# Kernel tuning notes

Hardware: AMD Instinct MI355X
Metric: run time of the kernel (lower is better)

The kernel has to match this reference:

```python
import jax, jax.numpy as jnp
import numpy as np

D = 768
H = 12
B, T = 2, 2048


def _layernorm(x, g, b, eps=1e-5):
    m = jnp.mean(x, axis=-1, keepdims=True)
    v = jnp.mean((x - m) ** 2, axis=-1, keepdims=True)
    return (x - m) * jax.lax.rsqrt(v + eps) * g + b


def setup_inputs() -> dict:
    key = jax.random.key(0)
    ks = jax.random.split(key, 10)
    s = 0.02
    return {
        "x": jax.random.normal(ks[0], (B, T, D), dtype=jnp.float32),
        "attn_mask": jnp.ones((B, T), dtype=jnp.int32),
        "Wq": jax.random.normal(ks[1], (D, D), dtype=jnp.float32) * s,
        "Wk": jax.random.normal(ks[2], (D, D), dtype=jnp.float32) * s,
        "Wv": jax.random.normal(ks[3], (D, D), dtype=jnp.float32) * s,
        "Wo": jax.random.normal(ks[4], (D, D), dtype=jnp.float32) * s,
        "bo": jnp.zeros((D,), dtype=jnp.float32),
        "ln1_g": jnp.ones((D,), dtype=jnp.float32),
        "ln1_b": jnp.zeros((D,), dtype=jnp.float32),
        "ln2_g": jnp.ones((D,), dtype=jnp.float32),
        "ln2_b": jnp.zeros((D,), dtype=jnp.float32),
        "W1": jax.random.normal(ks[5], (D, 4 * D), dtype=jnp.float32) * s,
        "b1": jnp.zeros((4 * D,), dtype=jnp.float32),
        "W2": jax.random.normal(ks[6], (4 * D, D), dtype=jnp.float32) * s,
        "b2": jnp.zeros((D,), dtype=jnp.float32),
    }


def reference(x, attn_mask, Wq, Wk, Wv, Wo, bo, ln1_g, ln1_b, ln2_g, ln2_b, W1, b1, W2, b2):
    d = x.shape[-1]
    hs = d // H
    # --- multi-head self-attention on ln1(x) ---
    h = _layernorm(x, ln1_g, ln1_b)
    q = jnp.einsum("btd,dhk->bhtk", h, Wq.reshape(d, H, hs))
    k = jnp.einsum("btd,dhk->bhtk", h, Wk.reshape(d, H, hs))
    v = jnp.einsum("btd,dhk->bhtk", h, Wv.reshape(d, H, hs))
    # NOTE: original scales by embed_dim**-0.5 (C = embed_dim), not head_size
    scores = jnp.einsum("bhtk,bhsk->bhts", q, k) * (d ** -0.5)
    key_mask = (attn_mask == 0)[:, None, None, :]  # [B,1,1,T] over key dim
    scores = jnp.where(key_mask, -jnp.inf, scores)
    wei = jax.nn.softmax(scores, axis=-1)
    out = jnp.einsum("bhts,bhsk->bhtk", wei, v)
    out = out.transpose(0, 2, 1, 3).reshape(x.shape)  # concat heads -> [B,T,D]
    x = x + out @ Wo + bo
    # --- feed-forward on ln2(x) ---
    h2 = _layernorm(x, ln2_g, ln2_b)
    ff = jax.nn.relu(h2 @ W1 + b1) @ W2 + b2
    return x + ff
```

## Files before the change

### kernel.cpp

```cpp
#include <hip/hip_runtime.h>


typedef unsigned short u16;
typedef unsigned int u32;
typedef __attribute__((ext_vector_type(8))) short s16x8;
typedef __attribute__((ext_vector_type(4))) float fx4;

#define D_MODEL 768
#define NH 12
#define HS 64
#define TT 2048
#define BB 2

__device__ __forceinline__ u16 f2bf(float f) {
  union { float f; u32 u; } v; v.f = f;
  u32 r = v.u + 0x7fffu + ((v.u >> 16) & 1u);
  return (u16)(r >> 16);
}
__device__ __forceinline__ float bf2f(u16 h) {
  union { u32 u; float f; } v; v.u = ((u32)h) << 16; return v.f;
}

__device__ __forceinline__ void async16(const void* g, void* l) {
  __builtin_amdgcn_global_load_lds(
      (const __attribute__((address_space(1))) u32*)g,
      (__attribute__((address_space(3))) u32*)l, 16, 0, 0);
}

__global__ __launch_bounds__(256) void tconv(const float* __restrict__ in,
                                             u16* __restrict__ out, int R, int C) {
  __shared__ float t[32][33];
  int c0 = blockIdx.x * 32, r0 = blockIdx.y * 32;
  int x = threadIdx.x, y = threadIdx.y;
  for (int i = 0; i < 4; i++)
    t[y + i * 8][x] = in[(size_t)(r0 + y + i * 8) * C + c0 + x];
  __syncthreads();
  for (int i = 0; i < 4; i++)
    out[(size_t)(c0 + y + i * 8) * R + r0 + x] = f2bf(t[x][y + i * 8]);
}

__global__ __launch_bounds__(256) void tconv3(const float* __restrict__ w0,
                                              const float* __restrict__ w1,
                                              const float* __restrict__ w2,
                                              u16* __restrict__ out) {
  __shared__ float t[32][33];
  const float* in = blockIdx.z == 0 ? w0 : blockIdx.z == 1 ? w1 : w2;
  u16* o = out + (size_t)blockIdx.z * 768 * 768;
  int c0 = blockIdx.x * 32, r0 = blockIdx.y * 32;
  int x = threadIdx.x, y = threadIdx.y;
  for (int i = 0; i < 4; i++)
    t[y + i * 8][x] = in[(size_t)(r0 + y + i * 8) * 768 + c0 + x];
  __syncthreads();
  for (int i = 0; i < 4; i++)
    o[(size_t)(c0 + y + i * 8) * 768 + r0 + x] = f2bf(t[x][y + i * 8]);
}

__global__ __launch_bounds__(256) void vt_extract(const u16* __restrict__ qkv,
                                                  u16* __restrict__ vt) {
  __shared__ u16 t[32][33];
  int bh = blockIdx.z, b = bh / NH, h = bh % NH;
  int t0 = blockIdx.x * 32, v0 = blockIdx.y * 32;
  int x = threadIdx.x, y = threadIdx.y;
  for (int i = 0; i < 4; i++)
    t[y + i * 8][x] = qkv[(size_t)(b * TT + t0 + y + i * 8) * 2304 + 1536 + h * HS + v0 + x];
  __syncthreads();
  for (int i = 0; i < 4; i++)
    vt[(size_t)(bh * HS + v0 + y + i * 8) * TT + t0 + x] = t[x][y + i * 8];
}

__global__ __launch_bounds__(256) void maskbias(const int* __restrict__ mask,
                                                float* __restrict__ mb) {
  int i = blockIdx.x * 256 + threadIdx.x;
  mb[i] = mask[i] ? 0.f : -1e30f;
}

__global__ __launch_bounds__(256) void ln_kernel(const float* __restrict__ x,
                                                 const float* __restrict__ g,
                                                 const float* __restrict__ bta,
                                                 u16* __restrict__ out) {
  int row = blockIdx.x;
  const float* xr = x + (size_t)row * D_MODEL;
  int tid = threadIdx.x;
  float v0 = xr[tid], v1 = xr[tid + 256], v2 = xr[tid + 512];
  float s = v0 + v1 + v2, sq = v0 * v0 + v1 * v1 + v2 * v2;
  for (int m = 1; m < 64; m <<= 1) { s += __shfl_xor(s, m); sq += __shfl_xor(sq, m); }
  __shared__ float ss[4], ssq[4];
  int w = tid >> 6;
  if ((tid & 63) == 0) { ss[w] = s; ssq[w] = sq; }
  __syncthreads();
  s = ss[0] + ss[1] + ss[2] + ss[3];
  sq = ssq[0] + ssq[1] + ssq[2] + ssq[3];
  float mean = s * (1.f / D_MODEL);
  float var = sq * (1.f / D_MODEL) - mean * mean;
  float rstd = rsqrtf(var + 1e-5f);
  u16* orow = out + (size_t)row * D_MODEL;
  orow[tid]       = f2bf((v0 - mean) * rstd * g[tid]       + bta[tid]);
  orow[tid + 256] = f2bf((v1 - mean) * rstd * g[tid + 256] + bta[tid + 256]);
  orow[tid + 512] = f2bf((v2 - mean) * rstd * g[tid + 512] + bta[tid + 512]);
}

__global__ __launch_bounds__(256) void red_wo_ln(
    const u16* __restrict__ p0, const u16* __restrict__ p1,
    const u16* __restrict__ p2, const u16* __restrict__ p3,
    const float* __restrict__ x, const float* __restrict__ bo,
    const float* __restrict__ g, const float* __restrict__ be,
    float* __restrict__ yv, u16* __restrict__ h2) {
  int row = blockIdx.x, tid = threadIdx.x;
  size_t base = (size_t)row * D_MODEL;
  float v[3];
  float s = 0.f, sq = 0.f;
  for (int i = 0; i < 3; i++) {
    int c = tid + i * 256;
    size_t idx = base + c;
    float t = bf2f(p0[idx]) + bf2f(p1[idx]) + bf2f(p2[idx]) + bf2f(p3[idx])
            + x[idx] + bo[c];
    v[i] = t; yv[idx] = t;
    s += t; sq += t * t;
  }
  for (int m = 1; m < 64; m <<= 1) { s += __shfl_xor(s, m); sq += __shfl_xor(sq, m); }
  __shared__ float ss[4], ssq[4];
  int w = tid >> 6;
  if ((tid & 63) == 0) { ss[w] = s; ssq[w] = sq; }
  __syncthreads();
  s = ss[0] + ss[1] + ss[2] + ss[3];
  sq = ssq[0] + ssq[1] + ssq[2] + ssq[3];
  float mean = s * (1.f / D_MODEL);
  float var = sq * (1.f / D_MODEL) - mean * mean;
  float rstd = rsqrtf(var + 1e-5f);
  for (int i = 0; i < 3; i++) {
    int c = tid + i * 256;
    h2[base + c] = f2bf((v[i] - mean) * rstd * g[c] + be[c]);
  }
}

__global__ __launch_bounds__(256) void red_ff2(
    const u16* __restrict__ p0, const u16* __restrict__ p1,
    const u16* __restrict__ p2, const float* __restrict__ yv,
    const float* __restrict__ bias, float* __restrict__ out) {
  size_t i = ((size_t)blockIdx.x * 256 + threadIdx.x) * 4;
  int col = (int)(i % D_MODEL);
  ushort4 a = *(const ushort4*)(p0 + i);
  ushort4 b = *(const ushort4*)(p1 + i);
  ushort4 c = *(const ushort4*)(p2 + i);
  float4 y = *(const float4*)(yv + i);
  float4 o;
  o.x = bf2f(a.x) + bf2f(b.x) + bf2f(c.x) + y.x + bias[col];
  o.y = bf2f(a.y) + bf2f(b.y) + bf2f(c.y) + y.y + bias[col + 1];
  o.z = bf2f(a.z) + bf2f(b.z) + bf2f(c.z) + y.z + bias[col + 2];
  o.w = bf2f(a.w) + bf2f(b.w) + bf2f(c.w) + y.w + bias[col + 3];
  *(float4*)(out + i) = o;
}

template <int EPI>
__global__ __launch_bounds__(256) void gemm_bt(
    const u16* __restrict__ A, const u16* __restrict__ Bt,
    int M, int N, int K,
    u16* __restrict__ outb, const float* __restrict__ bias,
    float qs, int qn,
    u16* __restrict__ p0, u16* __restrict__ p1,
    u16* __restrict__ p2, u16* __restrict__ p3) {
  __shared__ __align__(16) u16 lA[128 * 32];
  __shared__ __align__(16) u16 lB[128 * 32];
  const int tid = threadIdx.x;
  const int lane = tid & 63, w = tid >> 6;
  const int quad = lane >> 4, l15 = lane & 15;
  const int wm = w >> 1, wn = w & 1;
  const int bm = blockIdx.y, bn = blockIdx.x;
  const int Ksub = K / gridDim.z;
  const int k0 = blockIdx.z * Ksub;

  fx4 acc[4][4] = {};

  for (int kt = k0; kt < k0 + Ksub; kt += 32) {
    __syncthreads();
    for (int t = 0; t < 2; t++) {
      int p = (w * 2 + t) * 64 + lane;
      int m = p >> 2, qp = p & 3;
      int ql = qp ^ ((m >> 1) & 3);
      async16(A + (size_t)(bm * 128 + m) * K + kt + ql * 8,
              (char*)lA + (w * 2 + t) * 1024);
    }
    for (int t = 0; t < 2; t++) {
      int p = (w * 2 + t) * 64 + lane;
      int n = p >> 2, qp = p & 3;
      int ql = qp ^ ((n >> 1) & 3);
      async16(Bt + (size_t)(bn * 128 + n) * K + kt + ql * 8,
              (char*)lB + (w * 2 + t) * 1024);
    }
    __syncthreads();
    s16x8 af[4], bfr[4];
    for (int i = 0; i < 4; i++) {
      int m = wm * 64 + i * 16 + l15;
      int phys = m * 4 + (quad ^ ((m >> 1) & 3));
      af[i] = *(const s16x8*)((const char*)lA + phys * 16);
    }
    for (int j = 0; j < 4; j++) {
      int n = wn * 64 + j * 16 + l15;
      int phys = n * 4 + (quad ^ ((n >> 1) & 3));
      bfr[j] = *(const s16x8*)((const char*)lB + phys * 16);
    }
    for (int i = 0; i < 4; i++)
      for (int j = 0; j < 4; j++)
        acc[i][j] = __builtin_amdgcn_mfma_f32_16x16x32_bf16(af[i], bfr[j], acc[i][j], 0, 0, 0);
  }

  u16* pb = nullptr;
  if (EPI == 3)
    pb = blockIdx.z == 0 ? p0 : blockIdx.z == 1 ? p1 : blockIdx.z == 2 ? p2 : p3;

  for (int i = 0; i < 4; i++)
    for (int j = 0; j < 4; j++)
      for (int r = 0; r < 4; r++) {
        int row = bm * 128 + wm * 64 + i * 16 + quad * 4 + r;
        int col = bn * 128 + wn * 64 + j * 16 + l15;
        float v = acc[i][j][r];
        if (EPI == 0) {
          float vv = (col < qn) ? v * qs : v;
          outb[(size_t)row * N + col] = f2bf(vv);
        } else if (EPI == 2) {
          outb[(size_t)row * N + col] = f2bf(fmaxf(v + bias[col], 0.f));
        } else {
          pb[(size_t)row * N + col] = f2bf(v);
        }
      }
}

__global__ __launch_bounds__(256) void attn_kernel(
    const u16* __restrict__ qkv, const u16* __restrict__ vt,
    const float* __restrict__ maskadd, u16* __restrict__ out) {
  __shared__ __align__(16) u16 sQ[64 * 64];
  __shared__ __align__(16) u16 sK[64 * 64];
  __shared__ __align__(16) u16 sV[64 * 64];
  __shared__ __align__(16) u16 sP[4][16 * 64];
  const int bh = blockIdx.y, b = bh / NH, h = bh % NH;
  const int qt = blockIdx.x;
  const int tid = threadIdx.x, lane = tid & 63, w = tid >> 6;
  const int quad = lane >> 4, l15 = lane & 15;

  for (int t = 0; t < 2; t++) {
    int p = (w * 2 + t) * 64 + lane;
    int m = p >> 3, qp = p & 7, ql = qp ^ (m & 7);
    async16(qkv + (size_t)(b * TT + qt * 64 + m) * 2304 + h * HS + ql * 8,
            (char*)sQ + (w * 2 + t) * 1024);
  }
  __syncthreads();
  s16x8 aq[2];
  for (int kk = 0; kk < 2; kk++) {
    int m = w * 16 + l15;
    int phys = m * 8 + ((kk * 4 + quad) ^ (m & 7));
    aq[kk] = *(const s16x8*)((const char*)sQ + phys * 16);
  }

  float lsum[4] = {0.f, 0.f, 0.f, 0.f};
  fx4 o[4] = {};

  for (int kc = 0; kc < TT / 64; kc++) {
    __syncthreads();
    for (int t = 0; t < 2; t++) {
      int p = (w * 2 + t) * 64 + lane;
      int m = p >> 3, qp = p & 7, ql = qp ^ (m & 7);
      async16(qkv + (size_t)(b * TT + kc * 64 + m) * 2304 + D_MODEL + h * HS + ql * 8,
              (char*)sK + (w * 2 + t) * 1024);
    }
    for (int t = 0; t < 2; t++) {
      int p = (w * 2 + t) * 64 + lane;
      int m = p >> 3, qp = p & 7, ql = qp ^ (m & 7);
      async16(vt + (size_t)bh * HS * TT + (size_t)m * TT + kc * 64 + ql * 8,
              (char*)sV + (w * 2 + t) * 1024);
    }
    __syncthreads();

    for (int jn = 0; jn < 4; jn++) {
      float mb = maskadd[b * TT + kc * 64 + jn * 16 + l15];
      fx4 s = {mb, mb, mb, mb};
      for (int kk = 0; kk < 2; kk++) {
        int n = jn * 16 + l15;
        int phys = n * 8 + ((kk * 4 + quad) ^ (n & 7));
        s16x8 bk = *(const s16x8*)((const char*)sK + phys * 16);
        s = __builtin_amdgcn_mfma_f32_16x16x32_bf16(aq[kk], bk, s, 0, 0, 0);
      }
      for (int r = 0; r < 4; r++) {
        float p = __builtin_amdgcn_exp2f(s[r]);
        u16 pb = f2bf(p);
        lsum[r] += bf2f(pb);
        int row = quad * 4 + r, k = jn * 16 + l15;
        sP[w][row * 64 + ((k >> 3) ^ (row & 7)) * 8 + (k & 7)] = pb;
      }
    }
    for (int kk = 0; kk < 2; kk++) {
      int m = l15;
      int phys = m * 8 + ((kk * 4 + quad) ^ (m & 7));
      s16x8 ap = *(const s16x8*)((const char*)sP[w] + phys * 16);
      for (int jv = 0; jv < 4; jv++) {
        int n = jv * 16 + l15;
        int ph2 = n * 8 + ((kk * 4 + quad) ^ (n & 7));
        s16x8 bv = *(const s16x8*)((const char*)sV + ph2 * 16);
        o[jv] = __builtin_amdgcn_mfma_f32_16x16x32_bf16(ap, bv, o[jv], 0, 0, 0);
      }
    }
  }

  for (int mm = 1; mm < 16; mm <<= 1)
    for (int r = 0; r < 4; r++) lsum[r] += __shfl_xor(lsum[r], mm);

  for (int jv = 0; jv < 4; jv++)
    for (int r = 0; r < 4; r++) {
      int tok = qt * 64 + w * 16 + quad * 4 + r;
      out[(size_t)(b * TT + tok) * D_MODEL + h * HS + jv * 16 + l15] =
          f2bf(o[jv][r] / lsum[r]);
    }
}

extern "C" void kernel_launch(void* const* d_in, const int* in_sizes, int n_in,
                              void* d_out, int out_size, void* d_ws, size_t ws_size,
                              hipStream_t stream) {
  const float* x    = (const float*)d_in[0];
  const int*   mask = (const int*)d_in[1];
  const float* Wq   = (const float*)d_in[2];
  const float* Wk   = (const float*)d_in[3];
  const float* Wv   = (const float*)d_in[4];
  const float* Wo   = (const float*)d_in[5];
  const float* bo   = (const float*)d_in[6];
  const float* g1   = (const float*)d_in[7];
  const float* be1  = (const float*)d_in[8];
  const float* g2   = (const float*)d_in[9];
  const float* be2  = (const float*)d_in[10];
  const float* W1   = (const float*)d_in[11];
  const float* bb1  = (const float*)d_in[12];
  const float* W2   = (const float*)d_in[13];
  const float* bb2  = (const float*)d_in[14];
  float* out = (float*)d_out;
  char* ws = (char*)d_ws;

  u16*   WqkvT = (u16*)(ws + 0);
  u16*   WoT   = (u16*)(ws + 3538944);
  u16*   W1T   = (u16*)(ws + 4718592);
  u16*   W2T   = (u16*)(ws + 9437184);
  u16*   h1    = (u16*)(ws + 14155776);
  u16*   QKV   = (u16*)(ws + 20447232);
  u16*   Vt    = (u16*)(ws + 39321600);
  u16*   attn  = (u16*)(ws + 45613056);
  float* yv    = (float*)(ws + 51904512);
  float* mbias = yv;
  u16*   h2    = h1;
  u16*   ff1   = QKV;
  u16* pw0 = (u16*)(ws + 20447232);
  u16* pw1 = (u16*)(ws + 26738688);
  u16* pw2 = (u16*)(ws + 33030144);
  u16* pw3 = (u16*)(ws + 39321600);
  u16* pf0 = (u16*)(ws + 0);
  u16* pf1 = (u16*)(ws + 14155776);
  u16* pf2 = (u16*)(ws + 45613056);

  const float QS = 0.05205875399f;

  dim3 tb(32, 8);
  tconv3<<<dim3(24, 24, 3), tb, 0, stream>>>(Wq, Wk, Wv, WqkvT);
  tconv<<<dim3(24, 24), tb, 0, stream>>>(Wo, WoT, 768, 768);
  tconv<<<dim3(96, 24), tb, 0, stream>>>(W1, W1T, 768, 3072);
  tconv<<<dim3(24, 96), tb, 0, stream>>>(W2, W2T, 3072, 768);
  maskbias<<<16, 256, 0, stream>>>(mask, mbias);

  ln_kernel<<<4096, 256, 0, stream>>>(x, g1, be1, h1);
  gemm_bt<0><<<dim3(18, 32, 1), 256, 0, stream>>>(h1, WqkvT, 4096, 2304, 768,
      QKV, nullptr, QS, 768, nullptr, nullptr, nullptr, nullptr);
  vt_extract<<<dim3(64, 2, 24), tb, 0, stream>>>(QKV, Vt);
  attn_kernel<<<dim3(32, 24), 256, 0, stream>>>(QKV, Vt, mbias, attn);
  gemm_bt<3><<<dim3(6, 32, 4), 256, 0, stream>>>(attn, WoT, 4096, 768, 768,
      nullptr, nullptr, 1.f, 0, pw0, pw1, pw2, pw3);
  red_wo_ln<<<4096, 256, 0, stream>>>(pw0, pw1, pw2, pw3, x, bo, g2, be2, yv, h2);
  gemm_bt<2><<<dim3(24, 32, 1), 256, 0, stream>>>(h2, W1T, 4096, 3072, 768,
      ff1, bb1, 1.f, 0, nullptr, nullptr, nullptr, nullptr);
  gemm_bt<3><<<dim3(6, 32, 3), 256, 0, stream>>>(ff1, W2T, 4096, 768, 3072,
      nullptr, nullptr, 1.f, 0, pf0, pf1, pf2, nullptr);
  red_ff2<<<3072, 256, 0, stream>>>(pf0, pf1, pf2, yv, bb2, out);
}
```

Measured before the change: 319.2 us.

## Split attention over key halves and keep P in registers via transposed MFMA

The attention kernel is launched with a second grid dimension over two key halves, which doubles the block count, and each half writes unnormalized partial outputs and row sums. A new reduce kernel then combines and normalizes the halves and transposes the result into the token-major layout. The QK^T product is computed transposed with 16x16x16 bf16 MFMAs so the exponentiated scores feed the PV MFMA directly from registers, removing the shared-memory round trip for P. The mask is also staged in shared memory. The cost is an extra launch plus partial-output traffic, and bf16 rounding of the partial outputs before the sum.

Result: no change. 323.7 us (+1.4%).

```diff
diff --git a/kernel.cpp b/kernel.cpp
--- a/kernel.cpp
+++ b/kernel.cpp
@@ -1,9 +1,11 @@
 #include <hip/hip_runtime.h>
+#include <hip/hip_bf16.h>
 
 
 typedef unsigned short u16;
 typedef unsigned int u32;
 typedef __attribute__((ext_vector_type(8))) short s16x8;
+typedef __attribute__((ext_vector_type(4))) short s16x4;
 typedef __attribute__((ext_vector_type(4))) float fx4;
 
 #define D_MODEL 768
@@ -20,11 +22,22 @@
 __device__ __forceinline__ float bf2f(u16 h) {
   union { u32 u; float f; } v; v.u = ((u32)h) << 16; return v.f;
 }
+__device__ __forceinline__ s16x4 pack4(float a, float b, float c, float d) {
+  union { __hip_bfloat162 h2[2]; s16x4 v; } u;
+  u.h2[0] = __float22bfloat162_rn({a, b});
+  u.h2[1] = __float22bfloat162_rn({c, d});
+  return u.v;
+}
 
 __device__ __forceinline__ void async16(const void* g, void* l) {
   __builtin_amdgcn_global_load_lds(
       (const __attribute__((address_space(1))) u32*)g,
       (__attribute__((address_space(3))) u32*)l, 16, 0, 0);
+}
+
+__device__ __forceinline__ s16x4 lds_rd64(const u16* base, int row, int g) {
+  int a = row * 64 + ((((g >> 1) ^ (row & 7)) << 3) | ((g & 1) << 2));
+  return *(const s16x4*)(base + a);
 }
 
 __global__ __launch_bounds__(256) void tconv(const float* __restrict__ in,
@@ -227,13 +240,14 @@
 
 __global__ __launch_bounds__(256) void attn_kernel(
     const u16* __restrict__ qkv, const u16* __restrict__ vt,
-    const float* __restrict__ maskadd, u16* __restrict__ out) {
+    const float* __restrict__ maskadd,
+    u16* __restrict__ pO0, u16* __restrict__ pO1, float* __restrict__ pL) {
   __shared__ __align__(16) u16 sQ[64 * 64];
   __shared__ __align__(16) u16 sK[64 * 64];
   __shared__ __align__(16) u16 sV[64 * 64];
-  __shared__ __align__(16) u16 sP[4][16 * 64];
+  __shared__ __align__(16) float smask[1024];
   const int bh = blockIdx.y, b = bh / NH, h = bh % NH;
-  const int qt = blockIdx.x;
+  const int qt = blockIdx.x, sp = blockIdx.z;
   const int tid = threadIdx.x, lane = tid & 63, w = tid >> 6;
   const int quad = lane >> 4, l15 = lane & 15;
 
@@ -243,72 +257,91 @@
     async16(qkv + (size_t)(b * TT + qt * 64 + m) * 2304 + h * HS + ql * 8,
             (char*)sQ + (w * 2 + t) * 1024);
   }
-  __syncthreads();
-  s16x8 aq[2];
-  for (int kk = 0; kk < 2; kk++) {
-    int m = w * 16 + l15;
-    int phys = m * 8 + ((kk * 4 + quad) ^ (m & 7));
-    aq[kk] = *(const s16x8*)((const char*)sQ + phys * 16);
-  }
-
-  float lsum[4] = {0.f, 0.f, 0.f, 0.f};
+  for (int j = 0; j < 4; j++)
+    smask[tid + j * 256] = maskadd[b * TT + sp * 1024 + tid + j * 256];
+  __syncthreads();
+
+  s16x4 qb[4];
+  for (int ks = 0; ks < 4; ks++)
+    qb[ks] = lds_rd64(sQ, w * 16 + l15, ks * 4 + quad);
+
+  float lsum = 0.f;
   fx4 o[4] = {};
 
-  for (int kc = 0; kc < TT / 64; kc++) {
+  for (int kc = 0; kc < 16; kc++) {
+    int key0 = sp * 1024 + kc * 64;
     __syncthreads();
     for (int t = 0; t < 2; t++) {
       int p = (w * 2 + t) * 64 + lane;
       int m = p >> 3, qp = p & 7, ql = qp ^ (m & 7);
-      async16(qkv + (size_t)(b * TT + kc * 64 + m) * 2304 + D_MODEL + h * HS + ql * 8,
+      async16(qkv + (size_t)(b * TT + key0 + m) * 2304 + D_MODEL + h * HS + ql * 8,
               (char*)sK + (w * 2 + t) * 1024);
     }
     for (int t = 0; t < 2; t++) {
       int p = (w * 2 + t) * 64 + lane;
       int m = p >> 3, qp = p & 7, ql = qp ^ (m & 7);
-      async16(vt + (size_t)bh * HS * TT + (size_t)m * TT + kc * 64 + ql * 8,
+      async16(vt + (size_t)bh * HS * TT + (size_t)m * TT + key0 + ql * 8,
               (char*)sV + (w * 2 + t) * 1024);
     }
     __syncthreads();
 
-    for (int jn = 0; jn < 4; jn++) {
-      float mb = maskadd[b * TT + kc * 64 + jn * 16 + l15];
-      fx4 s = {mb, mb, mb, mb};
-      for (int kk = 0; kk < 2; kk++) {
-        int n = jn * 16 + l15;
-        int phys = n * 8 + ((kk * 4 + quad) ^ (n & 7));
-        s16x8 bk = *(const s16x8*)((const char*)sK + phys * 16);
-        s = __builtin_amdgcn_mfma_f32_16x16x32_bf16(aq[kk], bk, s, 0, 0, 0);
+    for (int kt = 0; kt < 4; kt++) {
+      float4 mb = *(const float4*)&smask[kc * 64 + kt * 16 + quad * 4];
+      fx4 s = {mb.x, mb.y, mb.z, mb.w};
+      for (int ks = 0; ks < 4; ks++) {
+        s16x4 ak = lds_rd64(sK, kt * 16 + l15, ks * 4 + quad);
+        s = __builtin_amdgcn_mfma_f32_16x16x16bf16_1k(ak, qb[ks], s, 0, 0, 0);
       }
-      for (int r = 0; r < 4; r++) {
-        float p = __builtin_amdgcn_exp2f(s[r]);
-        u16 pb = f2bf(p);
-        lsum[r] += bf2f(pb);
-        int row = quad * 4 + r, k = jn * 16 + l15;
-        sP[w][row * 64 + ((k >> 3) ^ (row & 7)) * 8 + (k & 7)] = pb;
+      float e0 = __builtin_amdgcn_exp2f(s[0]);
+      float e1 = __builtin_amdgcn_exp2f(s[1]);
+      float e2 = __builtin_amdgcn_exp2f(s[2]);
+      float e3 = __builtin_amdgcn_exp2f(s[3]);
+      lsum += (e0 + e1) + (e2 + e3);
+      s16x4 pB = pack4(e0, e1, e2, e3);
+      for (int jv = 0; jv < 4; jv++) {
+        s16x4 av = lds_rd64(sV, jv * 16 + l15, kt * 4 + quad);
+        o[jv] = __builtin_amdgcn_mfma_f32_16x16x16bf16_1k(av, pB, o[jv], 0, 0, 0);
       }
     }
-    for (int kk = 0; kk < 2; kk++) {
-      int m = l15;
-      int phys = m * 8 + ((kk * 4 + quad) ^ (m & 7));
-      s16x8 ap = *(const s16x8*)((const char*)sP[w] + phys * 16);
-      for (int jv = 0; jv < 4; jv++) {
-        int n = jv * 16 + l15;
-        int ph2 = n * 8 + ((kk * 4 + quad) ^ (n & 7));
-        s16x8 bv = *(const s16x8*)((const char*)sV + ph2 * 16);
-        o[jv] = __builtin_amdgcn_mfma_f32_16x16x32_bf16(ap, bv, o[jv], 0, 0, 0);
-      }
-    }
-  }
-
-  for (int mm = 1; mm < 16; mm <<= 1)
-    for (int r = 0; r < 4; r++) lsum[r] += __shfl_xor(lsum[r], mm);
-
+  }
+
+  lsum += __shfl_xor(lsum, 16);
+  lsum += __shfl_xor(lsum, 32);
+
+  const int tile = bh * 32 + qt;
+  u16* po = sp ? pO1 : pO0;
+  size_t base = (size_t)tile * 4096;
   for (int jv = 0; jv < 4; jv++)
     for (int r = 0; r < 4; r++) {
-      int tok = qt * 64 + w * 16 + quad * 4 + r;
-      out[(size_t)(b * TT + tok) * D_MODEL + h * HS + jv * 16 + l15] =
-          f2bf(o[jv][r] / lsum[r]);
-    }
+      int vd = jv * 16 + quad * 4 + r;
+      po[base + vd * 64 + w * 16 + l15] = f2bf(o[jv][r]);
+    }
+  if (quad == 0) pL[sp * 49152 + tile * 64 + w * 16 + l15] = lsum;
+}
+
+__global__ __launch_bounds__(256) void attn_reduce(
+    const u16* __restrict__ pO0, const u16* __restrict__ pO1,
+    const float* __restrict__ pL, u16* __restrict__ out) {
+  __shared__ float T[64 * 65];
+  __shared__ float rinv[64];
+  const int tile = blockIdx.x;
+  const int bh = tile >> 5, qt = tile & 31, b = bh / NH, h = bh % NH;
+  const int t = threadIdx.x;
+  if (t < 64) rinv[t] = 1.f / (pL[tile * 64 + t] + pL[49152 + tile * 64 + t]);
+  __syncthreads();
+  size_t base = (size_t)tile * 4096;
+  for (int i = 0; i < 16; i++) {
+    int idx = i * 256 + t, vd = idx >> 6, q = idx & 63;
+    T[vd * 65 + q] = (bf2f(pO0[base + idx]) + bf2f(pO1[base + idx])) * rinv[q];
+  }
+  __syncthreads();
+  int q = t >> 2, vb = (t & 3) * 16;
+  u16* orow = out + (size_t)(b * TT + qt * 64 + q) * D_MODEL + h * HS + vb;
+  for (int i = 0; i < 8; i++) {
+    int vd = vb + i * 2;
+    u32 pk = (u32)f2bf(T[vd * 65 + q]) | ((u32)f2bf(T[(vd + 1) * 65 + q]) << 16);
+    *(u32*)(orow + i * 2) = pk;
+  }
 }
 
 extern "C" void kernel_launch(void* const* d_in, const int* in_sizes, int n_in,
@@ -342,6 +375,9 @@
   u16*   attn  = (u16*)(ws + 45613056);
   float* yv    = (float*)(ws + 51904512);
   float* mbias = yv;
+  u16*   pO0   = h1;
+  u16*   pO1   = (u16*)(ws + 51920896);
+  float* pL    = (float*)(ws + 58212352);
   u16*   h2    = h1;
   u16*   ff1   = QKV;
   u16* pw0 = (u16*)(ws + 20447232);
@@ -365,7 +401,8 @@
   gemm_bt<0><<<dim3(18, 32, 1), 256, 0, stream>>>(h1, WqkvT, 4096, 2304, 768,
       QKV, nullptr, QS, 768, nullptr, nullptr, nullptr, nullptr);
   vt_extract<<<dim3(64, 2, 24), tb, 0, stream>>>(QKV, Vt);
-  attn_kernel<<<dim3(32, 24), 256, 0, stream>>>(QKV, Vt, mbias, attn);
+  attn_kernel<<<dim3(32, 24, 2), 256, 0, stream>>>(QKV, Vt, mbias, pO0, pO1, pL);
+  attn_reduce<<<768, 256, 0, stream>>>(pO0, pO1, pL, attn);
   gemm_bt<3><<<dim3(6, 32, 4), 256, 0, stream>>>(attn, WoT, 4096, 768, 768,
       nullptr, nullptr, 1.f, 0, pw0, pw1, pw2, pw3);
   red_wo_ln<<<4096, 256, 0, stream>>>(pw0, pw1, pw2, pw3, x, bo, g2, be2, yv, h2);
```
